# Optimization experiments

Measured on AMD Instinct MI355X. Metric: run time of the kernel, lower is better.

Reference implementation:

```python
import jax, jax.numpy as jnp
import numpy as np

K = 10  # topk classes


def setup_inputs() -> dict:
    key = jax.random.key(0)
    ks = jax.random.split(key, 12)
    B, DF, M, C, V, DW, DT = 64, 768, 26, 3129, 10000, 300, 1024
    s = lambda k, sh, scale: jax.random.normal(k, sh, dtype=jnp.float32) * scale
    return {
        "ftm": s(ks[0], (B, DF, M, M), 1.0),
        "logits": s(ks[1], (B, C), 1.0),
        "labels": jax.random.randint(ks[2], (B,), 0, C, dtype=jnp.int32),
        "indices_table": jax.random.randint(ks[3], (C, 4), 0, V, dtype=jnp.int32),
        "word2vec": s(ks[4], (V, DW), 1.0),
        "W_emb": s(ks[5], (DW, DT), 1.0 / np.sqrt(DW)),
        "b_emb": jnp.zeros((DT,), jnp.float32),
        "W_cls": s(ks[6], (DT, DT), 1.0 / np.sqrt(DT)),
        "b_cls": jnp.zeros((DT,), jnp.float32),
        "W_v": s(ks[7], (DF, DT), 1.0 / np.sqrt(DF)),
        "b_v": jnp.zeros((DT,), jnp.float32),
        "W_bap": s(ks[8], (DT, DT), 1.0 / np.sqrt(DT)),
        "b_bap": jnp.zeros((DT,), jnp.float32),
        "W_fc": s(ks[9], (DT, K), 1.0 / np.sqrt(DT)),
        "b_fc": jnp.zeros((K,), jnp.float32),
    }


def reference(ftm, logits, labels, indices_table, word2vec,
              W_emb, b_emb, W_cls, b_cls, W_v, b_v, W_bap, b_bap, W_fc, b_fc):
    B, DF = ftm.shape[0], ftm.shape[1]
    C = logits.shape[1]
    # dispatch: topk classes, gather their word indices, embed
    _, topk_idx = jax.lax.top_k(logits, K)                  # [B, K]
    topk_cls = indices_table[topk_idx]                      # [B, K, 4]
    emb = word2vec[topk_cls].mean(axis=2)                   # [B, K, 300] (ClassEmbedding pooling)
    cls_emb = jax.nn.relu(emb @ W_emb + b_emb)              # [B, K, 1024]
    # SAC_BAP (dropouts in eval mode = identity)
    cls_emb = jax.nn.relu(cls_emb @ W_cls + b_cls)          # [B, K, 1024]
    f = ftm.reshape(B, DF, -1).transpose(0, 2, 1)           # [B, F, 768], F = m*m
    v = jax.nn.relu(f @ W_v + b_v)                          # [B, F, 1024]
    att_w_b_sfx = jnp.einsum('bfd,bkd->bfk', v, cls_emb)    # [B, F, K]
    att_w = jax.nn.softmax(att_w_b_sfx, axis=1)             # softmax over positions
    bap = jnp.einsum('bfd,bfk,bkd->bd', v, att_w, cls_emb)  # [B, 1024]
    bap = jax.nn.relu(bap @ W_bap + b_bap)                  # bap_emb_FC
    bap_logits = bap @ W_fc + b_fc                          # fc_new 1x1 conv -> [B, K]
    # combine: scatter topk logits into the full class space
    um = jnp.zeros((B, C), dtype=bap_logits.dtype)
    um = um.at[jnp.arange(B)[:, None], topk_idx].set(bap_logits)
    return um
```

## Files before the change

### kernel.cpp

```cpp
#include <hip/hip_runtime.h>
#include <hip/hip_bf16.h>

#define B_   64
#define C_   3129
#define K_   10
#define DF_  768
#define F_   676
#define DW_  300
#define DWP_ 320
#define DT_  1024
#define NSEG 13
#define FSEG 52

typedef __attribute__((ext_vector_type(8))) short short8;
typedef __attribute__((ext_vector_type(4))) float floatx4;

__device__ __forceinline__ void gload_lds16(const void* g, void* l) {
    __builtin_amdgcn_global_load_lds(
        (const __attribute__((address_space(1))) void*)g,
        (__attribute__((address_space(3))) void*)l, 16, 0, 0);
}

__global__ void topk_emb_kernel(const float* __restrict__ logits,
                                const int* __restrict__ indices_table,
                                const float* __restrict__ word2vec,
                                int* __restrict__ topk_idx,
                                __hip_bfloat16* __restrict__ emb) {
    __shared__ float vals[C_];
    __shared__ float red_v[256];
    __shared__ int   red_i[256];
    __shared__ int   sel[K_];
    int b = blockIdx.x;
    int tid = threadIdx.x;
    for (int i = tid; i < C_; i += 256) vals[i] = logits[(size_t)b * C_ + i];
    __syncthreads();
    for (int s = 0; s < K_; ++s) {
        float bv = -INFINITY; int bi = 0x7fffffff;
        for (int i = tid; i < C_; i += 256) {
            float v = vals[i];
            if (v > bv) { bv = v; bi = i; }
        }
        red_v[tid] = bv; red_i[tid] = bi;
        __syncthreads();
        for (int st = 128; st > 0; st >>= 1) {
            if (tid < st) {
                float ov = red_v[tid + st]; int oi = red_i[tid + st];
                if (ov > red_v[tid] || (ov == red_v[tid] && oi < red_i[tid])) {
                    red_v[tid] = ov; red_i[tid] = oi;
                }
            }
            __syncthreads();
        }
        if (tid == 0) {
            sel[s] = red_i[0];
            topk_idx[b * K_ + s] = red_i[0];
            vals[red_i[0]] = -INFINITY;
        }
        __syncthreads();
    }
    for (int idx = tid; idx < K_ * DWP_; idx += 256) {
        int j  = idx % DWP_;
        int kk = idx / DWP_;
        float s = 0.f;
        if (j < DW_) {
            const int* tbl = indices_table + (size_t)sel[kk] * 4;
            #pragma unroll
            for (int i = 0; i < 4; ++i) s += word2vec[(size_t)tbl[i] * DW_ + j];
            s *= 0.25f;
        }
        emb[((size_t)b * K_ + kk) * DWP_ + j] = (__hip_bfloat16)s;
    }
}

__device__ __forceinline__ void tp_body(const float* __restrict__ s,
                                        __hip_bfloat16* __restrict__ d,
                                        int R, int Cc, int Rp, int c0, int r0) {
    __shared__ float tile[64][65];
    int t = threadIdx.x;
    int cl = (t & 15) * 4;
    int rl = t >> 4;
    #pragma unroll
    for (int i = 0; i < 4; ++i) {
        int r = rl + i * 16;
        float4 v = make_float4(0.f, 0.f, 0.f, 0.f);
        if (r0 + r < R && c0 + cl < Cc)
            v = *(const float4*)(s + (size_t)(r0 + r) * Cc + c0 + cl);
        tile[r][cl + 0] = v.x; tile[r][cl + 1] = v.y;
        tile[r][cl + 2] = v.z; tile[r][cl + 3] = v.w;
    }
    __syncthreads();
    int cw = t >> 2;
    int r4 = (t & 3) * 16;
    if (c0 + cw < Cc) {
        __align__(16) __hip_bfloat16 buf[16];
        #pragma unroll
        for (int j = 0; j < 16; ++j) buf[j] = (__hip_bfloat16)tile[r4 + j][cw];
        float4* dp = (float4*)(d + (size_t)(c0 + cw) * Rp + r0 + r4);
        dp[0] = *(float4*)&buf[0];
        dp[1] = *(float4*)&buf[8];
    }
}

__global__ __launch_bounds__(256)
void transpose_ftm(const float* __restrict__ src, __hip_bfloat16* __restrict__ dst) {
    tp_body(src + (size_t)blockIdx.z * DF_ * F_,
            dst + (size_t)blockIdx.z * F_ * DF_,
            DF_, F_, DF_, blockIdx.x * 64, blockIdx.y * 64);
}

__global__ __launch_bounds__(256)
void transpose_weights(const float* __restrict__ Wemb, __hip_bfloat16* __restrict__ WembT,
                       const float* __restrict__ Wcls, __hip_bfloat16* __restrict__ WclsT,
                       const float* __restrict__ Wv,   __hip_bfloat16* __restrict__ WvT,
                       const float* __restrict__ Wbap, __hip_bfloat16* __restrict__ WbapT) {
    int id = blockIdx.x;
    const float* s; __hip_bfloat16* d; int R, Rp;
    if (id < 80)       { s = Wemb; d = WembT; R = DW_;  Rp = DWP_; }
    else if (id < 336) { s = Wcls; d = WclsT; R = DT_;  Rp = DT_;  id -= 80;  }
    else if (id < 528) { s = Wv;   d = WvT;   R = DF_;  Rp = DF_;  id -= 336; }
    else               { s = Wbap; d = WbapT; R = DT_;  Rp = DT_;  id -= 528; }
    int bx = id & 15;
    int by = id >> 4;
    tp_body(s, d, R, DT_, Rp, bx * 64, by * 64);
}

__global__ __launch_bounds__(256)
void transpose_all(const float* __restrict__ Wemb, __hip_bfloat16* __restrict__ WembT,
                   const float* __restrict__ Wcls, __hip_bfloat16* __restrict__ WclsT,
                   const float* __restrict__ Wv,   __hip_bfloat16* __restrict__ WvT,
                   const float* __restrict__ Wbap, __hip_bfloat16* __restrict__ WbapT,
                   const float* __restrict__ ftm,  __hip_bfloat16* __restrict__ ftm_t) {
    int id = blockIdx.x;
    if (id >= 784) {
        id -= 784;
        int z = id / 132;
        int t2 = id % 132;
        int bx = t2 % 11, by = t2 / 11;
        tp_body(ftm + (size_t)z * DF_ * F_, ftm_t + (size_t)z * F_ * DF_,
                DF_, F_, DF_, bx * 64, by * 64);
        return;
    }
    const float* s; __hip_bfloat16* d; int R, Rp;
    if (id < 80)       { s = Wemb; d = WembT; R = DW_;  Rp = DWP_; }
    else if (id < 336) { s = Wcls; d = WclsT; R = DT_;  Rp = DT_;  id -= 80;  }
    else if (id < 528) { s = Wv;   d = WvT;   R = DF_;  Rp = DF_;  id -= 336; }
    else               { s = Wbap; d = WbapT; R = DT_;  Rp = DT_;  id -= 528; }
    int bx = id & 15;
    int by = id >> 4;
    tp_body(s, d, R, DT_, Rp, bx * 64, by * 64);
}

template <int RELU, int OUTBF>
__global__ __launch_bounds__(256)
void gemm_mfma(const __hip_bfloat16* __restrict__ A,
               const __hip_bfloat16* __restrict__ Bt,
               const float* __restrict__ bias,
               void* __restrict__ Cout, int M, int N, int Kp) {
    __shared__ __align__(16) char smem[34816];
    __hip_bfloat16* As = (__hip_bfloat16*)smem;
    __hip_bfloat16* Bs = As + 128 * 64;
    int tid = threadIdx.x;
    int wave = tid >> 6, lane = tid & 63;
    int quad = lane >> 4, l16 = lane & 15;
    int wm = (wave & 1) * 64, wn = (wave >> 1) * 64;

    int gx = gridDim.x;
    int nwg = gx * gridDim.y;
    int flat = blockIdx.y * gx + blockIdx.x;
    int q = nwg >> 3, r = nwg & 7;
    int xcd = flat & 7, lid = flat >> 3;
    int o = (xcd < r ? xcd * (q + 1) : r * (q + 1) + (xcd - r) * q) + lid;
    int n0 = (o % gx) * 128;
    int m0 = (o / gx) * 128;

    floatx4 acc[4][4];
    #pragma unroll
    for (int i = 0; i < 4; ++i)
        #pragma unroll
        for (int j = 0; j < 4; ++j)
            acc[i][j] = (floatx4){0.f, 0.f, 0.f, 0.f};

    int rsub = lane >> 3;
    int gchunk = (lane & 7) ^ rsub;

    int arow[4], brow[4];
    #pragma unroll
    for (int i = 0; i < 4; ++i) {
        arow[i] = wm + i * 16 + l16;
        brow[i] = wn + i * 16 + l16;
    }

    for (int k0 = 0; k0 < Kp; k0 += 64) {
        #pragma unroll
        for (int c = 0; c < 4; ++c) {
            int grp = wave * 4 + c;
            int row = grp * 8 + rsub;
            int ra = m0 + row; if (ra >= M) ra = M - 1;
            gload_lds16(A + (size_t)ra * Kp + k0 + gchunk * 8, As + grp * 512);
            gload_lds16(Bt + (size_t)(n0 + row) * Kp + k0 + gchunk * 8, Bs + grp * 512);
        }
        __syncthreads();
        #pragma unroll
        for (int ks = 0; ks < 2; ++ks) {
            short8 af[4], bf[4];
            #pragma unroll
            for (int mi = 0; mi < 4; ++mi)
                af[mi] = *(const short8*)&As[arow[mi] * 64 +
                            ((((ks << 2) | quad) ^ (arow[mi] & 7)) << 3)];
            #pragma unroll
            for (int ni = 0; ni < 4; ++ni)
                bf[ni] = *(const short8*)&Bs[brow[ni] * 64 +
                            ((((ks << 2) | quad) ^ (brow[ni] & 7)) << 3)];
            #pragma unroll
            for (int mi = 0; mi < 4; ++mi)
                #pragma unroll
                for (int ni = 0; ni < 4; ++ni)
                    acc[mi][ni] = __builtin_amdgcn_mfma_f32_16x16x32_bf16(
                        af[mi], bf[ni], acc[mi][ni], 0, 0, 0);
        }
        __syncthreads();
    }

    float bn[4];
    #pragma unroll
    for (int ni = 0; ni < 4; ++ni) bn[ni] = bias[n0 + wn + ni * 16 + l16];

    if (OUTBF) {
        __hip_bfloat16* Cs = (__hip_bfloat16*)smem;
        #pragma unroll
        for (int mi = 0; mi < 4; ++mi)
            #pragma unroll
            for (int rr = 0; rr < 4; ++rr) {
                int row = wm + mi * 16 + quad * 4 + rr;
                #pragma unroll
                for (int ni = 0; ni < 4; ++ni) {
                    float val = acc[mi][ni][rr] + bn[ni];
                    if (RELU) val = fmaxf(val, 0.f);
                    Cs[row * 136 + wn + ni * 16 + l16] = (__hip_bfloat16)val;
                }
            }
        __syncthreads();
        #pragma unroll
        for (int j = 0; j < 8; ++j) {
            int ch = tid + 256 * j;
            int row = ch >> 4, c16 = ch & 15;
            int r = m0 + row;
            float4 val = *(const float4*)&Cs[row * 136 + c16 * 8];
            if (r < M)
                *(float4*)((__hip_bfloat16*)Cout + (size_t)r * N + n0 + c16 * 8) = val;
        }
    } else {
        #pragma unroll
        for (int mi = 0; mi < 4; ++mi)
            #pragma unroll
            for (int rr = 0; rr < 4; ++rr) {
                int r = m0 + wm + mi * 16 + quad * 4 + rr;
                if (r < M) {
                    #pragma unroll
                    for (int ni = 0; ni < 4; ++ni) {
                        float val = acc[mi][ni][rr] + bn[ni];
                        if (RELU) val = fmaxf(val, 0.f);
                        ((float*)Cout)[(size_t)r * N + n0 + wn + ni * 16 + l16] = val;
                    }
                }
            }
    }
}

__global__ __launch_bounds__(256)
void attn_s_kernel(const __hip_bfloat16* __restrict__ v_buf,
                   const __hip_bfloat16* __restrict__ cls,
                   float* __restrict__ s_buf, int b0) {
    int tid = threadIdx.x;
    int wave = tid >> 6, lane = tid & 63;
    int bc = blockIdx.y;
    int f0 = blockIdx.x * 8 + wave * 2;
    int fa = f0 < F_ ? f0 : F_ - 1;
    int fb = (f0 + 1) < F_ ? f0 + 1 : F_ - 1;
    union U { float4 f4; __hip_bfloat16 h[8]; };
    const float4* va = (const float4*)(v_buf + ((size_t)(bc * F_ + fa)) * DT_ + lane * 16);
    const float4* vb = (const float4*)(v_buf + ((size_t)(bc * F_ + fb)) * DT_ + lane * 16);
    U a0, a1, b0u, b1u;
    a0.f4 = va[0]; a1.f4 = va[1];
    b0u.f4 = vb[0]; b1u.f4 = vb[1];
    float av[16], bv[16];
    #pragma unroll
    for (int i = 0; i < 8; ++i) {
        av[i] = (float)a0.h[i]; av[8 + i] = (float)a1.h[i];
        bv[i] = (float)b0u.h[i]; bv[8 + i] = (float)b1u.h[i];
    }
    const __hip_bfloat16* cp = cls + ((size_t)(b0 + bc) * K_) * DT_ + lane * 16;
    #pragma unroll
    for (int k = 0; k < K_; ++k) {
        const float4* c4 = (const float4*)(cp + (size_t)k * DT_);
        U c0u, c1u; c0u.f4 = c4[0]; c1u.f4 = c4[1];
        float da = 0.f, db = 0.f;
        #pragma unroll
        for (int i = 0; i < 8; ++i) {
            float cl0 = (float)c0u.h[i], cl1 = (float)c1u.h[i];
            da += av[i] * cl0 + av[8 + i] * cl1;
            db += bv[i] * cl0 + bv[8 + i] * cl1;
        }
        #pragma unroll
        for (int off = 32; off > 0; off >>= 1) {
            da += __shfl_down(da, off);
            db += __shfl_down(db, off);
        }
        if (lane == 0) {
            if (f0 < F_)     s_buf[((size_t)(bc * F_) + f0) * K_ + k] = da;
            if (f0 + 1 < F_) s_buf[((size_t)(bc * F_) + f0 + 1) * K_ + k] = db;
        }
    }
}

__global__ __launch_bounds__(256)
void o_bap_partial(const __hip_bfloat16* __restrict__ v_buf,
                   const float* __restrict__ s_buf,
                   const __hip_bfloat16* __restrict__ cls,
                   float* __restrict__ pp, int b0) {
    int bc = blockIdx.x, seg = blockIdx.y;
    int b = b0 + bc;
    int t = threadIdx.x;
    int f0 = seg * FSEG;
    __shared__ float wbuf[FSEG * K_];
    __shared__ float mk[K_], rlk[K_];
    __shared__ float red[128 * 8];

    if (t < 16 * K_) {
        int k = t >> 4, fi = t & 15;
        const float* sp = s_buf + (size_t)bc * F_ * K_ + k;
        float m = -INFINITY;
        for (int f = fi; f < F_; f += 16) m = fmaxf(m, sp[(size_t)f * K_]);
        #pragma unroll
        for (int off = 8; off > 0; off >>= 1) m = fmaxf(m, __shfl_xor(m, off, 16));
        float l = 0.f;
        for (int f = fi; f < F_; f += 16) l += __expf(sp[(size_t)f * K_] - m);
        #pragma unroll
        for (int off = 8; off > 0; off >>= 1) l += __shfl_xor(l, off, 16);
        if (fi == 0) { mk[k] = m; rlk[k] = 1.f / l; }
    }
    __syncthreads();
    for (int j = t; j < FSEG * K_; j += 256) {
        int k = j % K_;
        float sv = s_buf[((size_t)bc * F_ + f0) * K_ + j];
        wbuf[j] = __expf(sv - mk[k]) * rlk[k];
    }
    __syncthreads();
    int th = t & 127, half = t >> 7;
    int d0 = th * 8;
    int fs = half * (FSEG / 2);
    float acc[K_][8] = {};
    const __hip_bfloat16* vp = v_buf + ((size_t)bc * F_ + f0 + fs) * DT_ + d0;
    for (int f = 0; f < FSEG / 2; ++f) {
        union { float4 f4; __hip_bfloat16 h[8]; } u;
        u.f4 = *(const float4*)(vp + (size_t)f * DT_);
        float vv[8];
        #pragma unroll
        for (int i = 0; i < 8; ++i) vv[i] = (float)u.h[i];
        const float* wk = &wbuf[(fs + f) * K_];
        #pragma unroll
        for (int k = 0; k < K_; ++k)
            #pragma unroll
            for (int i = 0; i < 8; ++i) acc[k][i] += wk[k] * vv[i];
    }
    float outv[8] = {};
    union { float4 f4; __hip_bfloat16 h[8]; } cu;
    #pragma unroll
    for (int k = 0; k < K_; ++k) {
        cu.f4 = *(const float4*)(cls + ((size_t)b * K_ + k) * DT_ + d0);
        #pragma unroll
        for (int i = 0; i < 8; ++i) outv[i] += acc[k][i] * (float)cu.h[i];
    }
    if (half == 1) {
        *(float4*)&red[th * 8]     = *(float4*)&outv[0];
        *(float4*)&red[th * 8 + 4] = *(float4*)&outv[4];
    }
    __syncthreads();
    if (half == 0) {
        #pragma unroll
        for (int i = 0; i < 8; ++i) outv[i] += red[th * 8 + i];
        float* pd = pp + ((size_t)seg * B_ + b) * DT_ + d0;
        *(float4*)pd       = *(float4*)&outv[0];
        *(float4*)(pd + 4) = *(float4*)&outv[4];
    }
}

__global__ void bap_combine(const float* __restrict__ pp,
                            __hip_bfloat16* __restrict__ bap) {
    int idx = blockIdx.x * 256 + threadIdx.x;
    float s = 0.f;
    #pragma unroll
    for (int g = 0; g < NSEG; ++g) s += pp[idx + (size_t)g * B_ * DT_];
    bap[idx] = (__hip_bfloat16)s;
}

__global__ void final_kernel(const float* __restrict__ y,
                             const float* __restrict__ Wfc,
                             const float* __restrict__ bfc,
                             const int* __restrict__ topk_idx,
                             float* __restrict__ out) {
    int b = blockIdx.x, tid = threadIdx.x;
    int lane = tid & 63, wave = tid >> 6;
    float pk[K_] = {};
    for (int d = tid; d < DT_; d += 256) {
        float yv = y[(size_t)b * DT_ + d];
        #pragma unroll
        for (int k = 0; k < K_; ++k) pk[k] += yv * Wfc[(size_t)d * K_ + k];
    }
    __shared__ float wsum[4][K_];
    #pragma unroll
    for (int k = 0; k < K_; ++k) {
        float a = pk[k];
        #pragma unroll
        for (int off = 32; off > 0; off >>= 1) a += __shfl_down(a, off);
        if (lane == 0) wsum[wave][k] = a;
    }
    __syncthreads();
    if (tid < K_) {
        float lg = wsum[0][tid] + wsum[1][tid] + wsum[2][tid] + wsum[3][tid] + bfc[tid];
        out[(size_t)b * C_ + topk_idx[b * K_ + tid]] = lg;
    }
}

extern "C" void kernel_launch(void* const* d_in, const int* in_sizes, int n_in,
                              void* d_out, int out_size, void* d_ws, size_t ws_size,
                              hipStream_t stream) {
    const float* ftm           = (const float*)d_in[0];
    const float* logits        = (const float*)d_in[1];
    const int*   indices_table = (const int*)d_in[3];
    const float* word2vec      = (const float*)d_in[4];
    const float* W_emb         = (const float*)d_in[5];
    const float* b_emb         = (const float*)d_in[6];
    const float* W_cls         = (const float*)d_in[7];
    const float* b_cls         = (const float*)d_in[8];
    const float* W_v           = (const float*)d_in[9];
    const float* b_v           = (const float*)d_in[10];
    const float* W_bap         = (const float*)d_in[11];
    const float* b_bap         = (const float*)d_in[12];
    const float* W_fc          = (const float*)d_in[13];
    const float* b_fc          = (const float*)d_in[14];
    float* out = (float*)d_out;

    char* ws = (char*)d_ws;
    size_t off = 0;
    auto alloc = [&](size_t bytes) -> void* {
        void* p = ws + off;
        off = (off + bytes + 255) & ~(size_t)255;
        return p;
    };
    int*            topk_idx = (int*)           alloc((size_t)B_ * K_ * 4);
    __hip_bfloat16* emb_bf   = (__hip_bfloat16*)alloc((size_t)B_ * K_ * DWP_ * 2);
    __hip_bfloat16* cls1     = (__hip_bfloat16*)alloc((size_t)B_ * K_ * DT_ * 2);
    __hip_bfloat16* cls2     = (__hip_bfloat16*)alloc((size_t)B_ * K_ * DT_ * 2);
    __hip_bfloat16* Wemb_t   = (__hip_bfloat16*)alloc((size_t)DT_ * DWP_ * 2);
    __hip_bfloat16* Wcls_t   = (__hip_bfloat16*)alloc((size_t)DT_ * DT_ * 2);
    __hip_bfloat16* Wv_t     = (__hip_bfloat16*)alloc((size_t)DT_ * DF_ * 2);
    __hip_bfloat16* Wbap_t   = (__hip_bfloat16*)alloc((size_t)DT_ * DT_ * 2);
    float*          s_buf    = (float*)         alloc((size_t)B_ * F_ * K_ * 4);
    float*          pp       = (float*)         alloc((size_t)NSEG * B_ * DT_ * 4);
    __hip_bfloat16* bap_bf   = (__hip_bfloat16*)alloc((size_t)B_ * DT_ * 2);
    float*          yb       = (float*)         alloc((size_t)B_ * DT_ * 4);

    size_t per_b = (size_t)F_ * DF_ * 2 + (size_t)F_ * DT_ * 2;
    size_t avail = (ws_size > off + 8192) ? ws_size - off - 8192 : 0;
    int nb = (int)(avail / per_b);
    if (nb > B_) nb = B_;
    if (nb < 1) nb = 1;
    __hip_bfloat16* ftm_t = (__hip_bfloat16*)alloc((size_t)nb * F_ * DF_ * 2);
    __hip_bfloat16* v_buf = (__hip_bfloat16*)alloc((size_t)nb * F_ * DT_ * 2);

    hipMemsetAsync(d_out, 0, (size_t)out_size * sizeof(float), stream);

    topk_emb_kernel<<<B_, 256, 0, stream>>>(logits, indices_table, word2vec,
                                            topk_idx, emb_bf);

    if (nb == B_) {
        transpose_all<<<784 + 132 * B_, 256, 0, stream>>>(
            W_emb, Wemb_t, W_cls, Wcls_t, W_v, Wv_t, W_bap, Wbap_t, ftm, ftm_t);
    } else {
        transpose_weights<<<784, 256, 0, stream>>>(
            W_emb, Wemb_t, W_cls, Wcls_t, W_v, Wv_t, W_bap, Wbap_t);
    }

    gemm_mfma<1, 1><<<dim3(DT_ / 128, (B_ * K_ + 127) / 128), 256, 0, stream>>>(
        emb_bf, Wemb_t, b_emb, cls1, B_ * K_, DT_, DWP_);
    gemm_mfma<1, 1><<<dim3(DT_ / 128, (B_ * K_ + 127) / 128), 256, 0, stream>>>(
        cls1, Wcls_t, b_cls, cls2, B_ * K_, DT_, DT_);

    for (int b0 = 0; b0 < B_; b0 += nb) {
        int cb = min(nb, B_ - b0);
        if (nb != B_) {
            transpose_ftm<<<dim3((F_ + 63) / 64, DF_ / 64, cb), 256, 0, stream>>>(
                ftm + (size_t)b0 * DF_ * F_, ftm_t);
        }
        int M = cb * F_;
        gemm_mfma<1, 1><<<dim3(DT_ / 128, (M + 127) / 128), 256, 0, stream>>>(
            ftm_t, Wv_t, b_v, v_buf, M, DT_, DF_);
        float* s_c = s_buf + (size_t)b0 * F_ * K_;
        attn_s_kernel<<<dim3((F_ + 7) / 8, cb), 256, 0, stream>>>(
            v_buf, cls2, s_c, b0);
        o_bap_partial<<<dim3(cb, NSEG), 256, 0, stream>>>(
            v_buf, s_c, cls2, pp, b0);
    }
    bap_combine<<<B_ * DT_ / 256, 256, 0, stream>>>(pp, bap_bf);

    gemm_mfma<1, 0><<<dim3(DT_ / 128, 1), 256, 0, stream>>>(
        bap_bf, Wbap_t, b_bap, yb, B_, DT_, DT_);
    final_kernel<<<B_, 256, 0, stream>>>(yb, W_fc, b_fc, topk_idx, out);
}
```

Before: 486.4 us.

## Compute attention scores with MFMA and hoist softmax stats into separate kernel

Replaces the scalar per-wave dot-product attention score kernel with an MFMA bf16 tiled GEMM that stages v and class-embedding tiles in swizzled LDS via global_load_lds. It also moves the per-(batch,k) softmax max and sum reduction out of o_bap_partial, where each of the 13 segment blocks redundantly recomputed it, into a small dedicated kernel whose results are read back. This cuts ALU and redundant reads, at the cost of one extra launch and padding the K dimension from 10 to 16 in the MFMA.

```diff
diff --git a/kernel.cpp b/kernel.cpp
--- a/kernel.cpp
+++ b/kernel.cpp
@@ -268,54 +268,96 @@
 }
 
 __global__ __launch_bounds__(256)
-void attn_s_kernel(const __hip_bfloat16* __restrict__ v_buf,
-                   const __hip_bfloat16* __restrict__ cls,
-                   float* __restrict__ s_buf, int b0) {
+void attn_s_mfma(const __hip_bfloat16* __restrict__ v_buf,
+                 const __hip_bfloat16* __restrict__ cls,
+                 float* __restrict__ s_buf, int b0) {
+    __shared__ __align__(16) __hip_bfloat16 As[128 * 64];
+    __shared__ __align__(16) __hip_bfloat16 Bs[16 * 64];
     int tid = threadIdx.x;
     int wave = tid >> 6, lane = tid & 63;
+    int quad = lane >> 4, l16 = lane & 15;
     int bc = blockIdx.y;
-    int f0 = blockIdx.x * 8 + wave * 2;
-    int fa = f0 < F_ ? f0 : F_ - 1;
-    int fb = (f0 + 1) < F_ ? f0 + 1 : F_ - 1;
-    union U { float4 f4; __hip_bfloat16 h[8]; };
-    const float4* va = (const float4*)(v_buf + ((size_t)(bc * F_ + fa)) * DT_ + lane * 16);
-    const float4* vb = (const float4*)(v_buf + ((size_t)(bc * F_ + fb)) * DT_ + lane * 16);
-    U a0, a1, b0u, b1u;
-    a0.f4 = va[0]; a1.f4 = va[1];
-    b0u.f4 = vb[0]; b1u.f4 = vb[1];
-    float av[16], bv[16];
-    #pragma unroll
-    for (int i = 0; i < 8; ++i) {
-        av[i] = (float)a0.h[i]; av[8 + i] = (float)a1.h[i];
-        bv[i] = (float)b0u.h[i]; bv[8 + i] = (float)b1u.h[i];
-    }
-    const __hip_bfloat16* cp = cls + ((size_t)(b0 + bc) * K_) * DT_ + lane * 16;
-    #pragma unroll
-    for (int k = 0; k < K_; ++k) {
-        const float4* c4 = (const float4*)(cp + (size_t)k * DT_);
-        U c0u, c1u; c0u.f4 = c4[0]; c1u.f4 = c4[1];
-        float da = 0.f, db = 0.f;
-        #pragma unroll
-        for (int i = 0; i < 8; ++i) {
-            float cl0 = (float)c0u.h[i], cl1 = (float)c1u.h[i];
-            da += av[i] * cl0 + av[8 + i] * cl1;
-            db += bv[i] * cl0 + bv[8 + i] * cl1;
-        }
-        #pragma unroll
-        for (int off = 32; off > 0; off >>= 1) {
-            da += __shfl_down(da, off);
-            db += __shfl_down(db, off);
-        }
-        if (lane == 0) {
-            if (f0 < F_)     s_buf[((size_t)(bc * F_) + f0) * K_ + k] = da;
-            if (f0 + 1 < F_) s_buf[((size_t)(bc * F_) + f0 + 1) * K_ + k] = db;
-        }
-    }
+    int b = b0 + bc;
+    int f0 = blockIdx.x * 128;
+    int wm = wave * 32;
+
+    int rsub = lane >> 3;
+    int gchunk = (lane & 7) ^ rsub;
+
+    floatx4 acc[2];
+    acc[0] = (floatx4){0.f, 0.f, 0.f, 0.f};
+    acc[1] = (floatx4){0.f, 0.f, 0.f, 0.f};
+
+    int arow[2];
+    arow[0] = wm + l16;
+    arow[1] = wm + 16 + l16;
+
+    for (int k0 = 0; k0 < DT_; k0 += 64) {
+        #pragma unroll
+        for (int c = 0; c < 4; ++c) {
+            int grp = wave * 4 + c;
+            int row = grp * 8 + rsub;
+            int fa = f0 + row; if (fa >= F_) fa = F_ - 1;
+            gload_lds16(v_buf + ((size_t)bc * F_ + fa) * DT_ + k0 + gchunk * 8,
+                        As + grp * 512);
+        }
+        if (wave == 0) {
+            #pragma unroll
+            for (int c = 0; c < 2; ++c) {
+                int row = c * 8 + rsub;
+                int rc = row < K_ ? row : K_ - 1;
+                gload_lds16(cls + ((size_t)b * K_ + rc) * DT_ + k0 + gchunk * 8,
+                            Bs + c * 512);
+            }
+        }
+        __syncthreads();
+        #pragma unroll
+        for (int ks = 0; ks < 2; ++ks) {
+            short8 bf = *(const short8*)&Bs[l16 * 64 +
+                            ((((ks << 2) | quad) ^ (l16 & 7)) << 3)];
+            #pragma unroll
+            for (int mi = 0; mi < 2; ++mi) {
+                short8 af = *(const short8*)&As[arow[mi] * 64 +
+                                ((((ks << 2) | quad) ^ (arow[mi] & 7)) << 3)];
+                acc[mi] = __builtin_amdgcn_mfma_f32_16x16x32_bf16(
+                    af, bf, acc[mi], 0, 0, 0);
+            }
+        }
+        __syncthreads();
+    }
+
+    if (l16 < K_) {
+        #pragma unroll
+        for (int mi = 0; mi < 2; ++mi)
+            #pragma unroll
+            for (int rr = 0; rr < 4; ++rr) {
+                int f = f0 + wm + mi * 16 + quad * 4 + rr;
+                if (f < F_)
+                    s_buf[((size_t)bc * F_ + f) * K_ + l16] = acc[mi][rr];
+            }
+    }
+}
+
+__global__ __launch_bounds__(64)
+void softmax_stats(const float* __restrict__ s_buf, float2* __restrict__ ml,
+                   int b0) {
+    int k = blockIdx.x, bc = blockIdx.y, lane = threadIdx.x;
+    const float* sp = s_buf + (size_t)bc * F_ * K_ + k;
+    float m = -INFINITY;
+    for (int f = lane; f < F_; f += 64) m = fmaxf(m, sp[(size_t)f * K_]);
+    #pragma unroll
+    for (int off = 32; off > 0; off >>= 1) m = fmaxf(m, __shfl_xor(m, off));
+    float l = 0.f;
+    for (int f = lane; f < F_; f += 64) l += __expf(sp[(size_t)f * K_] - m);
+    #pragma unroll
+    for (int off = 32; off > 0; off >>= 1) l += __shfl_xor(l, off);
+    if (lane == 0) ml[(size_t)(b0 + bc) * K_ + k] = make_float2(m, 1.f / l);
 }
 
 __global__ __launch_bounds__(256)
 void o_bap_partial(const __hip_bfloat16* __restrict__ v_buf,
                    const float* __restrict__ s_buf,
+                   const float2* __restrict__ ml,
                    const __hip_bfloat16* __restrict__ cls,
                    float* __restrict__ pp, int b0) {
     int bc = blockIdx.x, seg = blockIdx.y;
@@ -325,19 +367,9 @@
     __shared__ float wbuf[FSEG * K_];
     __shared__ float mk[K_], rlk[K_];
     __shared__ float red[128 * 8];
-
-    if (t < 16 * K_) {
-        int k = t >> 4, fi = t & 15;
-        const float* sp = s_buf + (size_t)bc * F_ * K_ + k;
-        float m = -INFINITY;
-        for (int f = fi; f < F_; f += 16) m = fmaxf(m, sp[(size_t)f * K_]);
-        #pragma unroll
-        for (int off = 8; off > 0; off >>= 1) m = fmaxf(m, __shfl_xor(m, off, 16));
-        float l = 0.f;
-        for (int f = fi; f < F_; f += 16) l += __expf(sp[(size_t)f * K_] - m);
-        #pragma unroll
-        for (int off = 8; off > 0; off >>= 1) l += __shfl_xor(l, off, 16);
-        if (fi == 0) { mk[k] = m; rlk[k] = 1.f / l; }
+    if (t < K_) {
+        float2 v = ml[(size_t)b * K_ + t];
+        mk[t] = v.x; rlk[t] = v.y;
     }
     __syncthreads();
     for (int j = t; j < FSEG * K_; j += 256) {
@@ -457,6 +489,7 @@
     __hip_bfloat16* Wv_t     = (__hip_bfloat16*)alloc((size_t)DT_ * DF_ * 2);
     __hip_bfloat16* Wbap_t   = (__hip_bfloat16*)alloc((size_t)DT_ * DT_ * 2);
     float*          s_buf    = (float*)         alloc((size_t)B_ * F_ * K_ * 4);
+    float2*         ml       = (float2*)        alloc((size_t)B_ * K_ * 8);
     float*          pp       = (float*)         alloc((size_t)NSEG * B_ * DT_ * 4);
     __hip_bfloat16* bap_bf   = (__hip_bfloat16*)alloc((size_t)B_ * DT_ * 2);
     float*          yb       = (float*)         alloc((size_t)B_ * DT_ * 4);
@@ -497,10 +530,11 @@
         gemm_mfma<1, 1><<<dim3(DT_ / 128, (M + 127) / 128), 256, 0, stream>>>(
             ftm_t, Wv_t, b_v, v_buf, M, DT_, DF_);
         float* s_c = s_buf + (size_t)b0 * F_ * K_;
-        attn_s_kernel<<<dim3((F_ + 7) / 8, cb), 256, 0, stream>>>(
+        attn_s_mfma<<<dim3((F_ + 127) / 128, cb), 256, 0, stream>>>(
             v_buf, cls2, s_c, b0);
+        softmax_stats<<<dim3(K_, cb), 64, 0, stream>>>(s_c, ml, b0);
         o_bap_partial<<<dim3(cb, NSEG), 256, 0, stream>>>(
-            v_buf, s_c, cls2, pp, b0);
+            v_buf, s_c, ml, cls2, pp, b0);
     }
     bap_combine<<<B_ * DT_ / 256, 256, 0, stream>>>(pp, bap_bf);
 
```

Result: faster. 462.8 us (-4.8%).
